# Kernel tuning notes

Measured on AMD Instinct MI355X. Metric: run time of the kernel, lower is better.

The kernel has to match this reference:

```python
import jax, jax.numpy as jnp
import numpy as np

N = 50000      # nodes
E = 800000     # edges
IN = 256       # in_dim
H = 8          # heads
C = 32         # out_dim per head (H*C == IN so residual is identity)
NEG_SLOPE = 0.2
LN_EPS = 1e-5


def setup_inputs() -> dict:
    key = jax.random.key(0)
    ks = jax.random.split(key, 8)
    x = jax.random.normal(ks[0], (N, IN), dtype=jnp.float32)
    edge_index = jax.random.randint(ks[1], (2, E), 0, N, dtype=jnp.int64)
    # GATConv params
    W = jax.random.normal(ks[2], (IN, H * C), dtype=jnp.float32) / np.sqrt(IN)
    att_src = jax.random.normal(ks[3], (H, C), dtype=jnp.float32) / np.sqrt(C)
    att_dst = jax.random.normal(ks[4], (H, C), dtype=jnp.float32) / np.sqrt(C)
    bias = jnp.zeros((H * C,), dtype=jnp.float32)
    # LayerNorm params
    ln_scale = jnp.ones((H * C,), dtype=jnp.float32)
    ln_bias = jnp.zeros((H * C,), dtype=jnp.float32)
    return {"x": x, "edge_index": edge_index, "W": W, "att_src": att_src,
            "att_dst": att_dst, "bias": bias, "ln_scale": ln_scale, "ln_bias": ln_bias}


def _gat_block(x, edge_index, W, att_src, att_dst, bias, ln_scale, ln_bias):
    src, dst = edge_index[0], edge_index[1]
    # linear projection -> [N, H, C]
    h = (x @ W).reshape(N, H, C)
    # per-node attention logits [N, H]
    a_src = jnp.einsum('nhc,hc->nh', h, att_src)
    a_dst = jnp.einsum('nhc,hc->nh', h, att_dst)
    # per-edge logits with LeakyReLU [E, H]
    alpha = jax.nn.leaky_relu(a_src[src] + a_dst[dst], NEG_SLOPE)
    # segment softmax over incoming edges of each destination node
    amax = jax.ops.segment_max(alpha, dst, num_segments=N)          # [N, H]
    amax = jnp.where(jnp.isfinite(amax), amax, 0.0)                 # empty segments
    ex = jnp.exp(alpha - amax[dst])                                 # [E, H]
    denom = jax.ops.segment_sum(ex, dst, num_segments=N)           # [N, H]
    attn = ex / (denom[dst] + 1e-16)                                # [E, H]
    # weighted message aggregation -> [N, H, C]
    msg = h[src] * attn[:, :, None]
    out = jax.ops.segment_sum(msg, dst, num_segments=N)
    out = out.reshape(N, H * C) + bias
    # residual (identity since in_dim == heads*out_dim), ELU, LayerNorm
    out = out + x
    out = jax.nn.elu(out)
    mu = jnp.mean(out, axis=-1, keepdims=True)
    var = jnp.var(out, axis=-1, keepdims=True)
    return (out - mu) * jax.lax.rsqrt(var + LN_EPS) * ln_scale + ln_bias


def reference(x, edge_index, W, att_src, att_dst, bias, ln_scale, ln_bias):
    return _gat_block(x, edge_index, W, att_src, att_dst, bias, ln_scale, ln_bias)
```

## Files before the change

### kernel.cpp

```cpp
#include <hip/hip_runtime.h>
#include <hip/hip_bf16.h>
#include <cstdint>

#define NN 50000
#define NE 800000
#define DIM 256
#define NH 8
#define NB 196

typedef short v8s __attribute__((ext_vector_type(8)));
typedef float v4f __attribute__((ext_vector_type(4)));
typedef unsigned short u16x8 __attribute__((ext_vector_type(8)));

__device__ __forceinline__ float b2f(unsigned short u) {
    union { float f; uint32_t i; } c; c.i = ((uint32_t)u) << 16; return c.f;
}
__device__ __forceinline__ unsigned short f2b(float f) {
    union { float f; uint32_t i; } c; c.f = f;
    uint32_t lsb = (c.i >> 16) & 1u;
    return (unsigned short)((c.i + 0x7FFFu + lsb) >> 16);
}

__global__ __launch_bounds__(256) void deg_kernel(const int* __restrict__ e,
                                                  int* __restrict__ deg) {
    const int i = blockIdx.x * 256 + threadIdx.x;
    const int lane = threadIdx.x & 63;
    int probe = e[2 * lane + 1];
    unsigned long long nz = __ballot(probe != 0);
    bool is64 = (nz == 0ull);
    int d = is64 ? e[2 * (NE + i)] : e[NE + i];
    atomicAdd(&deg[d], 1);
}

__global__ __launch_bounds__(256) void cvtw_kernel(const float* __restrict__ W,
                                                   unsigned short* __restrict__ Wt) {
    int idx = blockIdx.x * 256 + threadIdx.x;
    int k = idx >> 8, n = idx & 255;
    Wt[n * DIM + k] = f2b(W[k * DIM + n]);
}

#define LDA3 72
__global__ __launch_bounds__(256) void gemm_kernel(
    const float* __restrict__ X, const unsigned short* __restrict__ Wt,
    unsigned short* __restrict__ H) {
    __shared__ __align__(16) unsigned short As[64 * LDA3];
    __shared__ __align__(16) unsigned short Bs[256 * LDA3];
    const int t = threadIdx.x;
    const int wc = t >> 6, lane = t & 63;
    const int fr = lane & 15, fq = lane >> 4;
    const int m0 = blockIdx.x * 64;

    v4f acc[4][4];
    #pragma unroll
    for (int mi = 0; mi < 4; ++mi)
        #pragma unroll
        for (int j = 0; j < 4; ++j) acc[mi][j] = (v4f){0.f, 0.f, 0.f, 0.f};

    #pragma unroll
    for (int kt = 0; kt < 256; kt += 64) {
        #pragma unroll
        for (int it = 0; it < 4; ++it) {
            int v = t + it * 256;
            int row = v >> 4;
            int c4 = (v & 15) << 2;
            int gr = m0 + row;
            float4 val = make_float4(0.f, 0.f, 0.f, 0.f);
            if (gr < NN) val = *(const float4*)(X + (size_t)gr * DIM + kt + c4);
            ushort4 o;
            o.x = f2b(val.x); o.y = f2b(val.y); o.z = f2b(val.z); o.w = f2b(val.w);
            *(ushort4*)(As + row * LDA3 + c4) = o;
        }
        #pragma unroll
        for (int it = 0; it < 8; ++it) {
            int v = t + it * 256;
            int row = v >> 3;
            int kv = (v & 7) << 3;
            u16x8 val = *(const u16x8*)(Wt + (size_t)row * DIM + kt + kv);
            *(u16x8*)(Bs + row * LDA3 + kv) = val;
        }
        __syncthreads();
        #pragma unroll
        for (int ks = 0; ks < 64; ks += 32) {
            v8s a[4];
            #pragma unroll
            for (int mi = 0; mi < 4; ++mi)
                a[mi] = *(const v8s*)(As + (mi * 16 + fr) * LDA3 + ks + fq * 8);
            #pragma unroll
            for (int j = 0; j < 4; ++j) {
                v8s b = *(const v8s*)(Bs + (wc * 64 + j * 16 + fr) * LDA3 + ks + fq * 8);
                #pragma unroll
                for (int mi = 0; mi < 4; ++mi)
                    acc[mi][j] = __builtin_amdgcn_mfma_f32_16x16x32_bf16(a[mi], b, acc[mi][j], 0, 0, 0);
            }
        }
        __syncthreads();
    }
    #pragma unroll
    for (int mi = 0; mi < 4; ++mi)
        #pragma unroll
        for (int j = 0; j < 4; ++j)
            #pragma unroll
            for (int r = 0; r < 4; ++r) {
                int gr = m0 + mi * 16 + fq * 4 + r;
                int gc = wc * 64 + j * 16 + fr;
                if (gr < NN) H[(size_t)gr * DIM + gc] = f2b(acc[mi][j][r]);
            }
}

__global__ __launch_bounds__(256) void att_kernel(
    const unsigned short* __restrict__ H, const float* __restrict__ ASRC,
    const float* __restrict__ ADST, float* __restrict__ a_src,
    float* __restrict__ a_dst) {
    const int wave = threadIdx.x >> 6, lane = threadIdx.x & 63;
    const int n = blockIdx.x * 4 + wave;
    if (n >= NN) return;
    float4 as4 = *(const float4*)(ASRC + lane * 4);
    float4 ad4 = *(const float4*)(ADST + lane * 4);
    ushort4 hv = *(const ushort4*)(H + (size_t)n * DIM + lane * 4);
    const unsigned short* hvp = (const unsigned short*)&hv;
    float h0 = b2f(hvp[0]), h1 = b2f(hvp[1]), h2 = b2f(hvp[2]), h3 = b2f(hvp[3]);
    float ps = h0 * as4.x + h1 * as4.y + h2 * as4.z + h3 * as4.w;
    float pd = h0 * ad4.x + h1 * ad4.y + h2 * ad4.z + h3 * ad4.w;
    #pragma unroll
    for (int off = 1; off <= 4; off <<= 1) {
        ps += __shfl_xor(ps, off);
        pd += __shfl_xor(pd, off);
    }
    if ((lane & 7) == 0) {
        a_src[n * NH + (lane >> 3)] = ps;
        a_dst[n * NH + (lane >> 3)] = pd;
    }
}

__global__ __launch_bounds__(256) void scan1_kernel(const int* __restrict__ deg,
                                                    int* __restrict__ row_start,
                                                    int* __restrict__ bsum) {
    const int t = threadIdx.x, b = blockIdx.x;
    const int i = b * 256 + t;
    const int lane = t & 63, wave = t >> 6;
    int v = (i < NN) ? deg[i] : 0;
    int x = v;
    #pragma unroll
    for (int off = 1; off <= 32; off <<= 1) {
        int y = __shfl_up(x, off);
        if (lane >= off) x += y;
    }
    __shared__ int wt[4];
    if (lane == 63) wt[wave] = x;
    __syncthreads();
    int add = 0;
    #pragma unroll
    for (int w2 = 0; w2 < 4; ++w2) if (w2 < wave) add += wt[w2];
    int incl = x + add;
    if (i < NN) row_start[i] = incl - v;
    if (t == 255) bsum[b] = incl;
}

__global__ __launch_bounds__(256) void scan2_kernel(const int* __restrict__ bsum,
                                                    int* __restrict__ boff,
                                                    int* __restrict__ row_start) {
    const int t = threadIdx.x;
    const int lane = t & 63, wave = t >> 6;
    int v = (t < NB) ? bsum[t] : 0;
    int x = v;
    #pragma unroll
    for (int off = 1; off <= 32; off <<= 1) {
        int y = __shfl_up(x, off);
        if (lane >= off) x += y;
    }
    __shared__ int wt[4];
    if (lane == 63) wt[wave] = x;
    __syncthreads();
    int add = 0;
    #pragma unroll
    for (int w2 = 0; w2 < 4; ++w2) if (w2 < wave) add += wt[w2];
    int incl = x + add;
    if (t < NB) boff[t] = incl - v;
    if (t == 255) row_start[NN] = incl;
}

__global__ __launch_bounds__(256) void scan3_kernel(int* __restrict__ row_start,
                                                    const int* __restrict__ boff,
                                                    int* __restrict__ cursor) {
    const int i = blockIdx.x * 256 + threadIdx.x;
    if (i < NN) {
        int r = row_start[i] + boff[blockIdx.x];
        row_start[i] = r;
        cursor[i] = r;
    }
}

__global__ __launch_bounds__(256) void fill_kernel(
    const int* __restrict__ e, const float* __restrict__ a_src,
    const float* __restrict__ a_dst, int* __restrict__ cursor,
    int* __restrict__ csr_src, float* __restrict__ wcsr) {
    const int i = blockIdx.x * 256 + threadIdx.x;
    const int lane = threadIdx.x & 63;
    int probe = e[2 * lane + 1];
    unsigned long long nz = __ballot(probe != 0);
    bool is64 = (nz == 0ull);
    int s, d;
    if (is64) { s = e[2 * i]; d = e[2 * (NE + i)]; }
    else      { s = e[i];     d = e[NE + i]; }
    int pos = atomicAdd(&cursor[d], 1);
    csr_src[pos] = s;
    float4 as0 = *(const float4*)(a_src + (size_t)s * NH);
    float4 as1 = *(const float4*)(a_src + (size_t)s * NH + 4);
    float4 ad0 = *(const float4*)(a_dst + (size_t)d * NH);
    float4 ad1 = *(const float4*)(a_dst + (size_t)d * NH + 4);
    const float* asp0 = (const float*)&as0; const float* asp1 = (const float*)&as1;
    const float* adp0 = (const float*)&ad0; const float* adp1 = (const float*)&ad1;
    float4 w0, w1;
    float* wp0 = (float*)&w0; float* wp1 = (float*)&w1;
    #pragma unroll
    for (int h = 0; h < 4; ++h) {
        float lg = asp0[h] + adp0[h];
        lg = lg > 0.f ? lg : 0.2f * lg;
        wp0[h] = __expf(lg);
        float lg2 = asp1[h] + adp1[h];
        lg2 = lg2 > 0.f ? lg2 : 0.2f * lg2;
        wp1[h] = __expf(lg2);
    }
    *(float4*)(wcsr + (size_t)pos * NH) = w0;
    *(float4*)(wcsr + (size_t)pos * NH + 4) = w1;
}

__global__ __launch_bounds__(256) void agg_kernel(
    const unsigned short* __restrict__ H, const int* __restrict__ row_start,
    const int* __restrict__ csr_src, const float* __restrict__ wcsr,
    const float* __restrict__ X, const float* __restrict__ BIAS,
    const float* __restrict__ LNS, const float* __restrict__ LNB,
    float* __restrict__ OUT) {
    const int wave = threadIdx.x >> 6, lane = threadIdx.x & 63;
    const int d = blockIdx.x * 4 + wave;
    if (d >= NN) return;
    const int base = row_start[d];
    const int degree = row_start[d + 1] - base;
    const int slot = lane >> 5;
    const int q = lane & 31;
    const int headq = q >> 2;

    float4 x0 = *(const float4*)(X + (size_t)d * DIM + q * 8);
    float4 x1 = *(const float4*)(X + (size_t)d * DIM + q * 8 + 4);
    float4 b0 = *(const float4*)(BIAS + q * 8);
    float4 b1 = *(const float4*)(BIAS + q * 8 + 4);
    float4 sc0 = *(const float4*)(LNS + q * 8);
    float4 sc1 = *(const float4*)(LNS + q * 8 + 4);
    float4 lb0 = *(const float4*)(LNB + q * 8);
    float4 lb1 = *(const float4*)(LNB + q * 8 + 4);

    float acc[8];
    #pragma unroll
    for (int j = 0; j < 8; ++j) acc[j] = 0.f;
    float sumw = 0.f;

    for (int c0 = 0; c0 < degree; c0 += 16) {
        const int e0 = c0 + slot * 8;
        const int rem = degree - e0;
        const size_t eb = (size_t)base + e0;
        int s[8]; float w[8];
        #pragma unroll
        for (int k = 0; k < 8; ++k) { s[k] = 0; w[k] = 0.f; }
        #pragma unroll
        for (int k = 0; k < 8; ++k)
            if (rem > k) { s[k] = csr_src[eb + k]; w[k] = wcsr[(eb + k) * NH + headq]; }
        u16x8 hv[8];
        #pragma unroll
        for (int k = 0; k < 8; ++k)
            hv[k] = *(const u16x8*)(H + (size_t)s[k] * DIM + q * 8);
        #pragma unroll
        for (int k = 0; k < 8; ++k) {
            sumw += w[k];
            #pragma unroll
            for (int j = 0; j < 8; ++j) acc[j] += w[k] * b2f(hv[k][j]);
        }
    }

    float sum_ex = sumw + __shfl_xor(sumw, 32);
    #pragma unroll
    for (int j = 0; j < 8; ++j) acc[j] += __shfl_xor(acc[j], 32);

    const float inv = 1.0f / (sum_ex + 1e-16f);

    const float* xp0 = (const float*)&x0; const float* xp1 = (const float*)&x1;
    const float* bp0 = (const float*)&b0; const float* bp1 = (const float*)&b1;
    float v[8];
    float s1v = 0.f, s2v = 0.f;
    #pragma unroll
    for (int j = 0; j < 8; ++j) {
        float xv = (j < 4) ? xp0[j] : xp1[j - 4];
        float bv = (j < 4) ? bp0[j] : bp1[j - 4];
        float t = acc[j] * inv + bv + xv;
        t = t > 0.f ? t : expm1f(t);
        v[j] = t;
        s1v += t;
        s2v += t * t;
    }
    #pragma unroll
    for (int off = 16; off >= 1; off >>= 1) {
        s1v += __shfl_xor(s1v, off);
        s2v += __shfl_xor(s2v, off);
    }
    const float mean = s1v * (1.0f / 256.0f);
    float var = s2v * (1.0f / 256.0f) - mean * mean;
    var = fmaxf(var, 0.f);
    const float rstd = rsqrtf(var + 1e-5f);

    if (slot == 0) {
        const float* scp0 = (const float*)&sc0; const float* scp1 = (const float*)&sc1;
        const float* lbp0 = (const float*)&lb0; const float* lbp1 = (const float*)&lb1;
        float4 o0, o1;
        float* op0 = (float*)&o0; float* op1 = (float*)&o1;
        #pragma unroll
        for (int j = 0; j < 4; ++j) {
            op0[j] = (v[j] - mean) * rstd * scp0[j] + lbp0[j];
            op1[j] = (v[j + 4] - mean) * rstd * scp1[j] + lbp1[j];
        }
        *(float4*)(OUT + (size_t)d * DIM + q * 8) = o0;
        *(float4*)(OUT + (size_t)d * DIM + q * 8 + 4) = o1;
    }
}

extern "C" void kernel_launch(void* const* d_in, const int* in_sizes, int n_in,
                              void* d_out, int out_size, void* d_ws, size_t ws_size,
                              hipStream_t stream) {
    const float* X    = (const float*)d_in[0];
    const int*   EIDX = (const int*)d_in[1];
    const float* W    = (const float*)d_in[2];
    const float* ASRC = (const float*)d_in[3];
    const float* ADST = (const float*)d_in[4];
    const float* BIAS = (const float*)d_in[5];
    const float* LNS  = (const float*)d_in[6];
    const float* LNB  = (const float*)d_in[7];
    float* OUT = (float*)d_out;

    char* ws = (char*)d_ws;
    unsigned short* H  = (unsigned short*)(ws);
    unsigned short* Wt = (unsigned short*)(ws + 25600000);
    float* a_srcW      = (float*)(ws + 25731072);
    float* a_dstW      = (float*)(ws + 27331072);
    int*   deg         = (int*)(ws + 28931072);
    int*   row_start   = (int*)(ws + 29131072);
    int*   cursor      = (int*)(ws + 29331088);
    int*   csr_src     = (int*)(ws + 29531088);
    float* wcsr        = (float*)(ws + 32731136);
    int*   bsum        = (int*)(ws + 58331136);
    int*   boff        = (int*)(ws + 58331920);

    hipMemsetAsync(deg, 0, NN * sizeof(int), stream);

    dim3 blk(256);
    deg_kernel<<<dim3(NE / 256), blk, 0, stream>>>(EIDX, deg);
    scan1_kernel<<<dim3(NB), blk, 0, stream>>>(deg, row_start, bsum);
    scan2_kernel<<<dim3(1), blk, 0, stream>>>(bsum, boff, row_start);
    scan3_kernel<<<dim3(NB), blk, 0, stream>>>(row_start, boff, cursor);
    cvtw_kernel<<<dim3(256), blk, 0, stream>>>(W, Wt);
    gemm_kernel<<<dim3(782), blk, 0, stream>>>(X, Wt, H);
    att_kernel<<<dim3((NN + 3) / 4), blk, 0, stream>>>(H, ASRC, ADST, a_srcW, a_dstW);
    fill_kernel<<<dim3(NE / 256), blk, 0, stream>>>(EIDX, a_srcW, a_dstW, cursor, csr_src, wcsr);
    agg_kernel<<<dim3((NN + 3) / 4), blk, 0, stream>>>(
        H, row_start, csr_src, wcsr, X, BIAS, LNS, LNB, OUT);
}
```

Baseline: 308.4 us.

## Fold attention projections into GEMM, fuse degree count, store edge weights as bf16

Precomputes W·att_src and W·att_dst as 16 extra bf16 columns of the transposed weight, so the GEMM emits the per-node attention logits with one extra MFMA tile on one wave. The separate att kernel, which re-read H, is removed. The degree-counting atomics move into the GEMM kernel prologue, and the deg kernel launch is dropped. Per-edge exp weights are stored as bf16 instead of fp32, halving that buffer's traffic in fill and aggregation, at some cost in precision of the logits and weights.

Result: slower. 320.6 us (+4.0%).

```diff
diff --git a/kernel.cpp b/kernel.cpp
--- a/kernel.cpp
+++ b/kernel.cpp
@@ -21,40 +21,69 @@
     return (unsigned short)((c.i + 0x7FFFu + lsb) >> 16);
 }
 
-__global__ __launch_bounds__(256) void deg_kernel(const int* __restrict__ e,
-                                                  int* __restrict__ deg) {
-    const int i = blockIdx.x * 256 + threadIdx.x;
-    const int lane = threadIdx.x & 63;
-    int probe = e[2 * lane + 1];
-    unsigned long long nz = __ballot(probe != 0);
-    bool is64 = (nz == 0ull);
-    int d = is64 ? e[2 * (NE + i)] : e[NE + i];
-    atomicAdd(&deg[d], 1);
-}
-
-__global__ __launch_bounds__(256) void cvtw_kernel(const float* __restrict__ W,
-                                                   unsigned short* __restrict__ Wt) {
-    int idx = blockIdx.x * 256 + threadIdx.x;
-    int k = idx >> 8, n = idx & 255;
-    Wt[n * DIM + k] = f2b(W[k * DIM + n]);
+__global__ __launch_bounds__(256) void prep_kernel(
+    const float* __restrict__ W, const float* __restrict__ ASRC,
+    const float* __restrict__ ADST, unsigned short* __restrict__ Wt) {
+    const int t = threadIdx.x;
+    if (blockIdx.x < 256) {
+        int idx = blockIdx.x * 256 + t;
+        int k = idx >> 8, n = idx & 255;
+        Wt[n * DIM + k] = f2b(W[k * DIM + n]);
+    } else {
+        const int k = t;
+        #pragma unroll
+        for (int h = 0; h < NH; ++h) {
+            float ss = 0.f, dd = 0.f;
+            #pragma unroll
+            for (int c4 = 0; c4 < 8; ++c4) {
+                float4 wv = *(const float4*)(W + (size_t)k * DIM + h * 32 + c4 * 4);
+                float4 av = *(const float4*)(ASRC + h * 32 + c4 * 4);
+                float4 dv = *(const float4*)(ADST + h * 32 + c4 * 4);
+                ss += wv.x * av.x + wv.y * av.y + wv.z * av.z + wv.w * av.w;
+                dd += wv.x * dv.x + wv.y * dv.y + wv.z * dv.z + wv.w * dv.w;
+            }
+            Wt[(256 + h) * DIM + k] = f2b(ss);
+            Wt[(264 + h) * DIM + k] = f2b(dd);
+        }
+    }
 }
 
 #define LDA3 72
 __global__ __launch_bounds__(256) void gemm_kernel(
     const float* __restrict__ X, const unsigned short* __restrict__ Wt,
-    unsigned short* __restrict__ H) {
+    const int* __restrict__ e, int* __restrict__ deg,
+    unsigned short* __restrict__ H, float* __restrict__ a_srcW,
+    float* __restrict__ a_dstW) {
     __shared__ __align__(16) unsigned short As[64 * LDA3];
-    __shared__ __align__(16) unsigned short Bs[256 * LDA3];
+    __shared__ __align__(16) unsigned short Bs[272 * LDA3];
     const int t = threadIdx.x;
     const int wc = t >> 6, lane = t & 63;
     const int fr = lane & 15, fq = lane >> 4;
     const int m0 = blockIdx.x * 64;
 
+    {
+        int probe = e[2 * lane + 1];
+        unsigned long long nz = __ballot(probe != 0);
+        bool is64 = (nz == 0ull);
+        int tg = blockIdx.x * 256 + t;
+        #pragma unroll
+        for (int j = 0; j < 4; ++j) {
+            int i = tg * 4 + j;
+            if (i < NE) {
+                int d = is64 ? e[2 * (NE + i)] : e[NE + i];
+                atomicAdd(&deg[d], 1);
+            }
+        }
+    }
+
     v4f acc[4][4];
-    #pragma unroll
-    for (int mi = 0; mi < 4; ++mi)
+    v4f acc4[4];
+    #pragma unroll
+    for (int mi = 0; mi < 4; ++mi) {
+        acc4[mi] = (v4f){0.f, 0.f, 0.f, 0.f};
         #pragma unroll
         for (int j = 0; j < 4; ++j) acc[mi][j] = (v4f){0.f, 0.f, 0.f, 0.f};
+    }
 
     #pragma unroll
     for (int kt = 0; kt < 256; kt += 64) {
@@ -71,12 +100,14 @@
             *(ushort4*)(As + row * LDA3 + c4) = o;
         }
         #pragma unroll
-        for (int it = 0; it < 8; ++it) {
+        for (int it = 0; it < 9; ++it) {
             int v = t + it * 256;
-            int row = v >> 3;
-            int kv = (v & 7) << 3;
-            u16x8 val = *(const u16x8*)(Wt + (size_t)row * DIM + kt + kv);
-            *(u16x8*)(Bs + row * LDA3 + kv) = val;
+            if (v < 2176) {
+                int row = v >> 3;
+                int kv = (v & 7) << 3;
+                u16x8 val = *(const u16x8*)(Wt + (size_t)row * DIM + kt + kv);
+                *(u16x8*)(Bs + row * LDA3 + kv) = val;
+            }
         }
         __syncthreads();
         #pragma unroll
@@ -92,6 +123,12 @@
                 for (int mi = 0; mi < 4; ++mi)
                     acc[mi][j] = __builtin_amdgcn_mfma_f32_16x16x32_bf16(a[mi], b, acc[mi][j], 0, 0, 0);
             }
+            if (wc == 0) {
+                v8s b4 = *(const v8s*)(Bs + (256 + fr) * LDA3 + ks + fq * 8);
+                #pragma unroll
+                for (int mi = 0; mi < 4; ++mi)
+                    acc4[mi] = __builtin_amdgcn_mfma_f32_16x16x32_bf16(a[mi], b4, acc4[mi], 0, 0, 0);
+            }
         }
         __syncthreads();
     }
@@ -105,30 +142,17 @@
                 int gc = wc * 64 + j * 16 + fr;
                 if (gr < NN) H[(size_t)gr * DIM + gc] = f2b(acc[mi][j][r]);
             }
-}
-
-__global__ __launch_bounds__(256) void att_kernel(
-    const unsigned short* __restrict__ H, const float* __restrict__ ASRC,
-    const float* __restrict__ ADST, float* __restrict__ a_src,
-    float* __restrict__ a_dst) {
-    const int wave = threadIdx.x >> 6, lane = threadIdx.x & 63;
-    const int n = blockIdx.x * 4 + wave;
-    if (n >= NN) return;
-    float4 as4 = *(const float4*)(ASRC + lane * 4);
-    float4 ad4 = *(const float4*)(ADST + lane * 4);
-    ushort4 hv = *(const ushort4*)(H + (size_t)n * DIM + lane * 4);
-    const unsigned short* hvp = (const unsigned short*)&hv;
-    float h0 = b2f(hvp[0]), h1 = b2f(hvp[1]), h2 = b2f(hvp[2]), h3 = b2f(hvp[3]);
-    float ps = h0 * as4.x + h1 * as4.y + h2 * as4.z + h3 * as4.w;
-    float pd = h0 * ad4.x + h1 * ad4.y + h2 * ad4.z + h3 * ad4.w;
-    #pragma unroll
-    for (int off = 1; off <= 4; off <<= 1) {
-        ps += __shfl_xor(ps, off);
-        pd += __shfl_xor(pd, off);
-    }
-    if ((lane & 7) == 0) {
-        a_src[n * NH + (lane >> 3)] = ps;
-        a_dst[n * NH + (lane >> 3)] = pd;
+    if (wc == 0) {
+        #pragma unroll
+        for (int mi = 0; mi < 4; ++mi)
+            #pragma unroll
+            for (int r = 0; r < 4; ++r) {
+                int gr = m0 + mi * 16 + fq * 4 + r;
+                if (gr < NN) {
+                    if (fr < 8) a_srcW[gr * NH + fr] = acc4[mi][r];
+                    else        a_dstW[gr * NH + (fr - 8)] = acc4[mi][r];
+                }
+            }
     }
 }
 
@@ -193,7 +217,7 @@
 __global__ __launch_bounds__(256) void fill_kernel(
     const int* __restrict__ e, const float* __restrict__ a_src,
     const float* __restrict__ a_dst, int* __restrict__ cursor,
-    int* __restrict__ csr_src, float* __restrict__ wcsr) {
+    int* __restrict__ csr_src, unsigned short* __restrict__ wcsr16) {
     const int i = blockIdx.x * 256 + threadIdx.x;
     const int lane = threadIdx.x & 63;
     int probe = e[2 * lane + 1];
@@ -210,24 +234,22 @@
     float4 ad1 = *(const float4*)(a_dst + (size_t)d * NH + 4);
     const float* asp0 = (const float*)&as0; const float* asp1 = (const float*)&as1;
     const float* adp0 = (const float*)&ad0; const float* adp1 = (const float*)&ad1;
-    float4 w0, w1;
-    float* wp0 = (float*)&w0; float* wp1 = (float*)&w1;
+    u16x8 wv;
     #pragma unroll
     for (int h = 0; h < 4; ++h) {
         float lg = asp0[h] + adp0[h];
         lg = lg > 0.f ? lg : 0.2f * lg;
-        wp0[h] = __expf(lg);
+        wv[h] = f2b(__expf(lg));
         float lg2 = asp1[h] + adp1[h];
         lg2 = lg2 > 0.f ? lg2 : 0.2f * lg2;
-        wp1[h] = __expf(lg2);
-    }
-    *(float4*)(wcsr + (size_t)pos * NH) = w0;
-    *(float4*)(wcsr + (size_t)pos * NH + 4) = w1;
+        wv[4 + h] = f2b(__expf(lg2));
+    }
+    *(u16x8*)(wcsr16 + (size_t)pos * NH) = wv;
 }
 
 __global__ __launch_bounds__(256) void agg_kernel(
     const unsigned short* __restrict__ H, const int* __restrict__ row_start,
-    const int* __restrict__ csr_src, const float* __restrict__ wcsr,
+    const int* __restrict__ csr_src, const unsigned short* __restrict__ wcsr16,
     const float* __restrict__ X, const float* __restrict__ BIAS,
     const float* __restrict__ LNS, const float* __restrict__ LNB,
     float* __restrict__ OUT) {
@@ -263,7 +285,10 @@
         for (int k = 0; k < 8; ++k) { s[k] = 0; w[k] = 0.f; }
         #pragma unroll
         for (int k = 0; k < 8; ++k)
-            if (rem > k) { s[k] = csr_src[eb + k]; w[k] = wcsr[(eb + k) * NH + headq]; }
+            if (rem > k) {
+                s[k] = csr_src[eb + k];
+                w[k] = b2f(wcsr16[(eb + k) * NH + headq]);
+            }
         u16x8 hv[8];
         #pragma unroll
         for (int k = 0; k < 8; ++k)
@@ -335,29 +360,27 @@
     float* OUT = (float*)d_out;
 
     char* ws = (char*)d_ws;
-    unsigned short* H  = (unsigned short*)(ws);
-    unsigned short* Wt = (unsigned short*)(ws + 25600000);
-    float* a_srcW      = (float*)(ws + 25731072);
-    float* a_dstW      = (float*)(ws + 27331072);
-    int*   deg         = (int*)(ws + 28931072);
-    int*   row_start   = (int*)(ws + 29131072);
-    int*   cursor      = (int*)(ws + 29331088);
-    int*   csr_src     = (int*)(ws + 29531088);
-    float* wcsr        = (float*)(ws + 32731136);
-    int*   bsum        = (int*)(ws + 58331136);
-    int*   boff        = (int*)(ws + 58331920);
+    unsigned short* H   = (unsigned short*)(ws);
+    unsigned short* Wt  = (unsigned short*)(ws + 25600000);
+    float* a_srcW       = (float*)(ws + 25739264);
+    float* a_dstW       = (float*)(ws + 27339264);
+    int*   deg          = (int*)(ws + 28939264);
+    int*   row_start    = (int*)(ws + 29139264);
+    int*   cursor       = (int*)(ws + 29339280);
+    int*   csr_src      = (int*)(ws + 29539280);
+    unsigned short* wcsr16 = (unsigned short*)(ws + 32739280);
+    int*   bsum         = (int*)(ws + 45539280);
+    int*   boff         = (int*)(ws + 45540064);
 
     hipMemsetAsync(deg, 0, NN * sizeof(int), stream);
 
     dim3 blk(256);
-    deg_kernel<<<dim3(NE / 256), blk, 0, stream>>>(EIDX, deg);
+    prep_kernel<<<dim3(257), blk, 0, stream>>>(W, ASRC, ADST, Wt);
+    gemm_kernel<<<dim3(782), blk, 0, stream>>>(X, Wt, EIDX, deg, H, a_srcW, a_dstW);
     scan1_kernel<<<dim3(NB), blk, 0, stream>>>(deg, row_start, bsum);
     scan2_kernel<<<dim3(1), blk, 0, stream>>>(bsum, boff, row_start);
     scan3_kernel<<<dim3(NB), blk, 0, stream>>>(row_start, boff, cursor);
-    cvtw_kernel<<<dim3(256), blk, 0, stream>>>(W, Wt);
-    gemm_kernel<<<dim3(782), blk, 0, stream>>>(X, Wt, H);
-    att_kernel<<<dim3((NN + 3) / 4), blk, 0, stream>>>(H, ASRC, ADST, a_srcW, a_dstW);
-    fill_kernel<<<dim3(NE / 256), blk, 0, stream>>>(EIDX, a_srcW, a_dstW, cursor, csr_src, wcsr);
+    fill_kernel<<<dim3(NE / 256), blk, 0, stream>>>(EIDX, a_srcW, a_dstW, cursor, csr_src, wcsr16);
     agg_kernel<<<dim3((NN + 3) / 4), blk, 0, stream>>>(
-        H, row_start, csr_src, wcsr, X, BIAS, LNS, LNB, OUT);
-}
+        H, row_start, csr_src, wcsr16, X, BIAS, LNS, LNB, OUT);
+}
```
